# Performance work log

Measured on AMD Instinct MI355X. Metric: run time of the kernel, lower is better.

## Reference

```python
import jax, jax.numpy as jnp
import numpy as np

B = 8192
N_CLASSES = 1024
MARGIN = 0.1
THRESH = 0.5
SCALE_POS = 2.0
SCALE_NEG = 40.0
EPS = 1e-5


def setup_inputs() -> dict:
    key = jax.random.key(0)
    k1, k2 = jax.random.split(key)
    # cosine-similarity-like values in [-1, 1]
    sim_mat = jax.random.uniform(k1, (B, B), dtype=jnp.float32, minval=-1.0, maxval=1.0)
    labels = jax.random.randint(k2, (B,), 0, N_CLASSES, dtype=jnp.int64)
    return {"sim_mat": sim_mat, "labels": labels}


def reference(sim_mat, labels):
    # [B, B] pair masks
    same = labels[:, None] == labels[None, :]
    pos_mask = same & (sim_mat < 1.0 - EPS)        # positives, excluding self-sim ~ 1
    neg_mask = ~same

    # per-row hardest positive (min) / hardest negative (max); inf sentinels when empty
    min_pos = jnp.min(jnp.where(pos_mask, sim_mat, jnp.inf), axis=1)   # [B]
    max_neg = jnp.max(jnp.where(neg_mask, sim_mat, -jnp.inf), axis=1)  # [B]

    # pair mining: keep informative pairs only
    sel_neg = neg_mask & (sim_mat + MARGIN > min_pos[:, None])
    sel_pos = pos_mask & (sim_mat - MARGIN < max_neg[:, None])

    valid = jnp.any(sel_neg, axis=1) & jnp.any(sel_pos, axis=1)  # rows contributing to loss

    # masked soft-plus style logsumexp losses (sim bounded in [-1,1], exp is safe)
    pos_sum = jnp.sum(jnp.where(sel_pos, jnp.exp(-SCALE_POS * (sim_mat - THRESH)), 0.0), axis=1)
    neg_sum = jnp.sum(jnp.where(sel_neg, jnp.exp(SCALE_NEG * (sim_mat - THRESH)), 0.0), axis=1)
    pos_loss = jnp.log1p(pos_sum) / SCALE_POS
    neg_loss = jnp.log1p(neg_sum) / SCALE_NEG

    loss = jnp.sum(jnp.where(valid, pos_loss + neg_loss, 0.0)) / sim_mat.shape[0]
    return loss
```

## Files before the change

kernel.cpp:

```cpp
#include <hip/hip_runtime.h>
#include <math.h>

namespace {
constexpr int   kB        = 8192;
constexpr int   kBlock    = 256;
constexpr int   kVec      = 4;
constexpr int   kIters    = kB / (kBlock * kVec);
constexpr float kMargin   = 0.1f;
constexpr float kThresh   = 0.5f;
constexpr float kScalePos = 2.0f;
constexpr float kScaleNeg = 40.0f;
constexpr float kEps      = 1e-5f;
}

__global__ __launch_bounds__(kBlock, 4) void ms_loss_kernel(
    const float* __restrict__ sim,
    const int*   __restrict__ labels,
    float*       __restrict__ out)
{
  const int row  = blockIdx.x;
  const int tid  = threadIdx.x;
  const int wave = tid >> 6;
  const int lane = tid & 63;

  const int my_label = labels[row];
  const float* __restrict__ srow = sim + (size_t)row * kB;

  float4 v[kIters];
  #pragma unroll
  for (int k = 0; k < kIters; ++k) {
    v[k] = *reinterpret_cast<const float4*>(srow + k * (kBlock * kVec) + tid * kVec);
  }

  unsigned int same_mask = 0;
  #pragma unroll
  for (int k = 0; k < kIters; ++k) {
    const int4 l = *reinterpret_cast<const int4*>(labels + k * (kBlock * kVec) + tid * kVec);
    same_mask |= (unsigned)(l.x == my_label) << (k * 4 + 0);
    same_mask |= (unsigned)(l.y == my_label) << (k * 4 + 1);
    same_mask |= (unsigned)(l.z == my_label) << (k * 4 + 2);
    same_mask |= (unsigned)(l.w == my_label) << (k * 4 + 3);
  }

  float min_pos =  INFINITY;
  float max_neg = -INFINITY;
  #pragma unroll
  for (int k = 0; k < kIters; ++k) {
    const float xs[4] = {v[k].x, v[k].y, v[k].z, v[k].w};
    #pragma unroll
    for (int c = 0; c < 4; ++c) {
      const bool  same = (same_mask >> (k * 4 + c)) & 1u;
      const float x = xs[c];
      const float p = (same && x < 1.0f - kEps) ? x : INFINITY;
      const float n = same ? -INFINITY : x;
      min_pos = fminf(min_pos, p);
      max_neg = fmaxf(max_neg, n);
    }
  }

  #pragma unroll
  for (int off = 32; off > 0; off >>= 1) {
    min_pos = fminf(min_pos, __shfl_xor(min_pos, off, 64));
    max_neg = fmaxf(max_neg, __shfl_xor(max_neg, off, 64));
  }
  __shared__ float s_min[kBlock / 64];
  __shared__ float s_max[kBlock / 64];
  if (lane == 0) { s_min[wave] = min_pos; s_max[wave] = max_neg; }
  __syncthreads();
  min_pos = fminf(fminf(s_min[0], s_min[1]), fminf(s_min[2], s_min[3]));
  max_neg = fmaxf(fmaxf(s_max[0], s_max[1]), fmaxf(s_max[2], s_max[3]));

  float pos_sum = 0.0f, neg_sum = 0.0f;
  #pragma unroll
  for (int k = 0; k < kIters; ++k) {
    const float xs[4] = {v[k].x, v[k].y, v[k].z, v[k].w};
    #pragma unroll
    for (int c = 0; c < 4; ++c) {
      const bool  same = (same_mask >> (k * 4 + c)) & 1u;
      const float x = xs[c];
      const float a = same ? -kScalePos : kScaleNeg;
      const float e = __expf(a * (x - kThresh));
      const bool selp = same && (x < 1.0f - kEps) && (x - kMargin < max_neg);
      const bool seln = (!same) && (x + kMargin > min_pos);
      pos_sum += selp ? e : 0.0f;
      neg_sum += seln ? e : 0.0f;
    }
  }

  #pragma unroll
  for (int off = 32; off > 0; off >>= 1) {
    pos_sum += __shfl_xor(pos_sum, off, 64);
    neg_sum += __shfl_xor(neg_sum, off, 64);
  }
  __shared__ float s_pos[kBlock / 64];
  __shared__ float s_neg[kBlock / 64];
  if (lane == 0) { s_pos[wave] = pos_sum; s_neg[wave] = neg_sum; }
  __syncthreads();
  if (tid == 0) {
    pos_sum = (s_pos[0] + s_pos[1]) + (s_pos[2] + s_pos[3]);
    neg_sum = (s_neg[0] + s_neg[1]) + (s_neg[2] + s_neg[3]);
    if (pos_sum > 0.0f && neg_sum > 0.0f) {
      const float loss = log1pf(pos_sum) * (1.0f / kScalePos)
                       + log1pf(neg_sum) * (1.0f / kScaleNeg);
      atomicAdd(out, loss * (1.0f / (float)kB));
    }
  }
}

extern "C" void kernel_launch(void* const* d_in, const int* in_sizes, int n_in,
                              void* d_out, int out_size, void* d_ws, size_t ws_size,
                              hipStream_t stream) {
  const float* sim    = (const float*)d_in[0];
  const int*   labels = (const int*)d_in[1];
  float*       out    = (float*)d_out;

  hipMemsetAsync(d_out, 0, sizeof(float) * (size_t)out_size, stream);
  ms_loss_kernel<<<dim3(kB), dim3(kBlock), 0, stream>>>(sim, labels, out);
}
```

Measured before the change: 377.6 us.

## Process eight rows per block with double-buffered row prefetch

Each block now handles eight consecutive rows instead of one. It loads the column labels once and builds a same-label bitmask for every row up front. While the current row is reduced, the next row of the similarity matrix is loaded into a second register buffer, so load latency overlaps the min/max and exp passes. The per-row losses are summed in the block and written with one atomic, cutting global atomics eightfold. The costs are a higher register footprint from the two float4 buffers and a grid of only 1024 blocks, which may reduce occupancy and latency hiding.

After: 371.2 us. Within noise of the previous version (-1.7%).

```diff
diff --git a/kernel.cpp b/kernel.cpp
--- a/kernel.cpp
+++ b/kernel.cpp
@@ -5,7 +5,9 @@
 constexpr int   kB        = 8192;
 constexpr int   kBlock    = 256;
 constexpr int   kVec      = 4;
-constexpr int   kIters    = kB / (kBlock * kVec);
+constexpr int   kChunks   = kB / (kBlock * kVec);
+constexpr int   kRows     = 8;
+constexpr int   kGrid     = kB / kRows;
 constexpr float kMargin   = 0.1f;
 constexpr float kThresh   = 0.5f;
 constexpr float kScalePos = 2.0f;
@@ -18,92 +20,118 @@
     const int*   __restrict__ labels,
     float*       __restrict__ out)
 {
-  const int row  = blockIdx.x;
-  const int tid  = threadIdx.x;
-  const int wave = tid >> 6;
-  const int lane = tid & 63;
+  const int tid      = threadIdx.x;
+  const int wave     = tid >> 6;
+  const int lane     = tid & 63;
+  const int base_row = blockIdx.x * kRows;
 
-  const int my_label = labels[row];
-  const float* __restrict__ srow = sim + (size_t)row * kB;
+  int4 lab[kChunks];
+  #pragma unroll
+  for (int k = 0; k < kChunks; ++k)
+    lab[k] = *reinterpret_cast<const int4*>(labels + k * (kBlock * kVec) + tid * kVec);
 
-  float4 v[kIters];
+  unsigned int mask[kRows];
   #pragma unroll
-  for (int k = 0; k < kIters; ++k) {
-    v[k] = *reinterpret_cast<const float4*>(srow + k * (kBlock * kVec) + tid * kVec);
+  for (int r = 0; r < kRows; ++r) {
+    const int ml = labels[base_row + r];
+    unsigned int m = 0;
+    #pragma unroll
+    for (int k = 0; k < kChunks; ++k) {
+      m |= (unsigned)(lab[k].x == ml) << (k * 4 + 0);
+      m |= (unsigned)(lab[k].y == ml) << (k * 4 + 1);
+      m |= (unsigned)(lab[k].z == ml) << (k * 4 + 2);
+      m |= (unsigned)(lab[k].w == ml) << (k * 4 + 3);
+    }
+    mask[r] = m;
   }
 
-  unsigned int same_mask = 0;
-  #pragma unroll
-  for (int k = 0; k < kIters; ++k) {
-    const int4 l = *reinterpret_cast<const int4*>(labels + k * (kBlock * kVec) + tid * kVec);
-    same_mask |= (unsigned)(l.x == my_label) << (k * 4 + 0);
-    same_mask |= (unsigned)(l.y == my_label) << (k * 4 + 1);
-    same_mask |= (unsigned)(l.z == my_label) << (k * 4 + 2);
-    same_mask |= (unsigned)(l.w == my_label) << (k * 4 + 3);
+  float4 buf[2][kChunks];
+  {
+    const float* __restrict__ s0 = sim + (size_t)base_row * kB;
+    #pragma unroll
+    for (int k = 0; k < kChunks; ++k)
+      buf[0][k] = *reinterpret_cast<const float4*>(s0 + k * (kBlock * kVec) + tid * kVec);
   }
 
-  float min_pos =  INFINITY;
-  float max_neg = -INFINITY;
+  __shared__ float s_min[kBlock / 64];
+  __shared__ float s_max[kBlock / 64];
+  __shared__ float s_pos[kBlock / 64];
+  __shared__ float s_neg[kBlock / 64];
+
+  float block_loss = 0.0f;
+
   #pragma unroll
-  for (int k = 0; k < kIters; ++k) {
-    const float xs[4] = {v[k].x, v[k].y, v[k].z, v[k].w};
+  for (int r = 0; r < kRows; ++r) {
+    if (r + 1 < kRows) {
+      const float* __restrict__ sn = sim + (size_t)(base_row + r + 1) * kB;
+      #pragma unroll
+      for (int k = 0; k < kChunks; ++k)
+        buf[(r + 1) & 1][k] =
+            *reinterpret_cast<const float4*>(sn + k * (kBlock * kVec) + tid * kVec);
+    }
+
+    const unsigned int m = mask[r];
+
+    float min_pos =  INFINITY;
+    float max_neg = -INFINITY;
     #pragma unroll
-    for (int c = 0; c < 4; ++c) {
-      const bool  same = (same_mask >> (k * 4 + c)) & 1u;
-      const float x = xs[c];
-      const float p = (same && x < 1.0f - kEps) ? x : INFINITY;
-      const float n = same ? -INFINITY : x;
-      min_pos = fminf(min_pos, p);
-      max_neg = fmaxf(max_neg, n);
+    for (int k = 0; k < kChunks; ++k) {
+      const float4 v = buf[r & 1][k];
+      const float xs[4] = {v.x, v.y, v.z, v.w};
+      #pragma unroll
+      for (int c = 0; c < 4; ++c) {
+        const bool  same = (m >> (k * 4 + c)) & 1u;
+        const float x = xs[c];
+        min_pos = fminf(min_pos, (same && x < 1.0f - kEps) ? x : INFINITY);
+        max_neg = fmaxf(max_neg, same ? -INFINITY : x);
+      }
+    }
+    #pragma unroll
+    for (int off = 32; off > 0; off >>= 1) {
+      min_pos = fminf(min_pos, __shfl_xor(min_pos, off, 64));
+      max_neg = fmaxf(max_neg, __shfl_xor(max_neg, off, 64));
+    }
+    if (lane == 0) { s_min[wave] = min_pos; s_max[wave] = max_neg; }
+    __syncthreads();
+    min_pos = fminf(fminf(s_min[0], s_min[1]), fminf(s_min[2], s_min[3]));
+    max_neg = fmaxf(fmaxf(s_max[0], s_max[1]), fmaxf(s_max[2], s_max[3]));
+
+    float pos_sum = 0.0f, neg_sum = 0.0f;
+    #pragma unroll
+    for (int k = 0; k < kChunks; ++k) {
+      const float4 v = buf[r & 1][k];
+      const float xs[4] = {v.x, v.y, v.z, v.w};
+      #pragma unroll
+      for (int c = 0; c < 4; ++c) {
+        const bool  same = (m >> (k * 4 + c)) & 1u;
+        const float x = xs[c];
+        const float a = same ? -kScalePos : kScaleNeg;
+        const float e = __expf(a * (x - kThresh));
+        const bool selp = same && (x < 1.0f - kEps) && (x - kMargin < max_neg);
+        const bool seln = (!same) && (x + kMargin > min_pos);
+        pos_sum += selp ? e : 0.0f;
+        neg_sum += seln ? e : 0.0f;
+      }
+    }
+    #pragma unroll
+    for (int off = 32; off > 0; off >>= 1) {
+      pos_sum += __shfl_xor(pos_sum, off, 64);
+      neg_sum += __shfl_xor(neg_sum, off, 64);
+    }
+    if (lane == 0) { s_pos[wave] = pos_sum; s_neg[wave] = neg_sum; }
+    __syncthreads();
+    if (tid == 0) {
+      pos_sum = (s_pos[0] + s_pos[1]) + (s_pos[2] + s_pos[3]);
+      neg_sum = (s_neg[0] + s_neg[1]) + (s_neg[2] + s_neg[3]);
+      if (pos_sum > 0.0f && neg_sum > 0.0f) {
+        block_loss += log1pf(pos_sum) * (1.0f / kScalePos)
+                    + log1pf(neg_sum) * (1.0f / kScaleNeg);
+      }
     }
   }
 
-  #pragma unroll
-  for (int off = 32; off > 0; off >>= 1) {
-    min_pos = fminf(min_pos, __shfl_xor(min_pos, off, 64));
-    max_neg = fmaxf(max_neg, __shfl_xor(max_neg, off, 64));
-  }
-  __shared__ float s_min[kBlock / 64];
-  __shared__ float s_max[kBlock / 64];
-  if (lane == 0) { s_min[wave] = min_pos; s_max[wave] = max_neg; }
-  __syncthreads();
-  min_pos = fminf(fminf(s_min[0], s_min[1]), fminf(s_min[2], s_min[3]));
-  max_neg = fmaxf(fmaxf(s_max[0], s_max[1]), fmaxf(s_max[2], s_max[3]));
-
-  float pos_sum = 0.0f, neg_sum = 0.0f;
-  #pragma unroll
-  for (int k = 0; k < kIters; ++k) {
-    const float xs[4] = {v[k].x, v[k].y, v[k].z, v[k].w};
-    #pragma unroll
-    for (int c = 0; c < 4; ++c) {
-      const bool  same = (same_mask >> (k * 4 + c)) & 1u;
-      const float x = xs[c];
-      const float a = same ? -kScalePos : kScaleNeg;
-      const float e = __expf(a * (x - kThresh));
-      const bool selp = same && (x < 1.0f - kEps) && (x - kMargin < max_neg);
-      const bool seln = (!same) && (x + kMargin > min_pos);
-      pos_sum += selp ? e : 0.0f;
-      neg_sum += seln ? e : 0.0f;
-    }
-  }
-
-  #pragma unroll
-  for (int off = 32; off > 0; off >>= 1) {
-    pos_sum += __shfl_xor(pos_sum, off, 64);
-    neg_sum += __shfl_xor(neg_sum, off, 64);
-  }
-  __shared__ float s_pos[kBlock / 64];
-  __shared__ float s_neg[kBlock / 64];
-  if (lane == 0) { s_pos[wave] = pos_sum; s_neg[wave] = neg_sum; }
-  __syncthreads();
-  if (tid == 0) {
-    pos_sum = (s_pos[0] + s_pos[1]) + (s_pos[2] + s_pos[3]);
-    neg_sum = (s_neg[0] + s_neg[1]) + (s_neg[2] + s_neg[3]);
-    if (pos_sum > 0.0f && neg_sum > 0.0f) {
-      const float loss = log1pf(pos_sum) * (1.0f / kScalePos)
-                       + log1pf(neg_sum) * (1.0f / kScaleNeg);
-      atomicAdd(out, loss * (1.0f / (float)kB));
-    }
+  if (tid == 0 && block_loss != 0.0f) {
+    atomicAdd(out, block_loss * (1.0f / (float)kB));
   }
 }
 
@@ -115,5 +143,5 @@
   float*       out    = (float*)d_out;
 
   hipMemsetAsync(d_out, 0, sizeof(float) * (size_t)out_size, stream);
-  ms_loss_kernel<<<dim3(kB), dim3(kBlock), 0, stream>>>(sim, labels, out);
+  ms_loss_kernel<<<dim3(kGrid), dim3(kBlock), 0, stream>>>(sim, labels, out);
 }
```

## Map rows to single waves and replace atomics with two-stage reduction

Applied to the files above, without the earlier changes.

Each 64-lane wave now owns whole rows, two per wave, and holds the 8192-float row in 32 float4 registers, so block-level shared-memory reductions and syncthreads are gone. Per-wave partial losses go to workspace and a second single-block kernel sums them, which replaces the memset plus 8192 atomics. The cost is much higher register pressure (launch bounds lowered to 2) and less memory-level parallelism per row. It also depends on a workspace buffer and adds a second launch.

Measured after the change: 432.9 us. 14.6% more time.

```diff
diff --git a/kernel.cpp b/kernel.cpp
--- a/kernel.cpp
+++ b/kernel.cpp
@@ -2,10 +2,13 @@
 #include <math.h>
 
 namespace {
-constexpr int   kB        = 8192;
-constexpr int   kBlock    = 256;
-constexpr int   kVec      = 4;
-constexpr int   kIters    = kB / (kBlock * kVec);
+constexpr int   kB       = 8192;
+constexpr int   kBlock   = 256;
+constexpr int   kWaves   = kBlock / 64;
+constexpr int   kRPW     = 2;
+constexpr int   kGrid    = kB / (kWaves * kRPW);
+constexpr int   kChunks  = kB / (64 * 4);
+constexpr int   kNWaves  = kGrid * kWaves;
 constexpr float kMargin   = 0.1f;
 constexpr float kThresh   = 0.5f;
 constexpr float kScalePos = 2.0f;
@@ -13,98 +16,96 @@
 constexpr float kEps      = 1e-5f;
 }
 
-__global__ __launch_bounds__(kBlock, 4) void ms_loss_kernel(
+__global__ __launch_bounds__(kBlock, 2) void ms_rows_kernel(
     const float* __restrict__ sim,
     const int*   __restrict__ labels,
-    float*       __restrict__ out)
+    float*       __restrict__ ws)
 {
-  const int row  = blockIdx.x;
   const int tid  = threadIdx.x;
   const int wave = tid >> 6;
   const int lane = tid & 63;
+  const int wid  = blockIdx.x * kWaves + wave;
 
-  const int my_label = labels[row];
-  const float* __restrict__ srow = sim + (size_t)row * kB;
+  float wave_loss = 0.0f;
 
-  float4 v[kIters];
   #pragma unroll
-  for (int k = 0; k < kIters; ++k) {
-    v[k] = *reinterpret_cast<const float4*>(srow + k * (kBlock * kVec) + tid * kVec);
-  }
+  for (int rr = 0; rr < kRPW; ++rr) {
+    const int row = wid * kRPW + rr;
+    const int ml  = labels[row];
+    const float* __restrict__ srow = sim + (size_t)row * kB;
 
-  unsigned int same_mask = 0;
-  #pragma unroll
-  for (int k = 0; k < kIters; ++k) {
-    const int4 l = *reinterpret_cast<const int4*>(labels + k * (kBlock * kVec) + tid * kVec);
-    same_mask |= (unsigned)(l.x == my_label) << (k * 4 + 0);
-    same_mask |= (unsigned)(l.y == my_label) << (k * 4 + 1);
-    same_mask |= (unsigned)(l.z == my_label) << (k * 4 + 2);
-    same_mask |= (unsigned)(l.w == my_label) << (k * 4 + 3);
-  }
+    float4 buf[kChunks];
+    #pragma unroll
+    for (int k = 0; k < kChunks; ++k)
+      buf[k] = *reinterpret_cast<const float4*>(srow + k * 256 + lane * 4);
 
-  float min_pos =  INFINITY;
-  float max_neg = -INFINITY;
-  #pragma unroll
-  for (int k = 0; k < kIters; ++k) {
-    const float xs[4] = {v[k].x, v[k].y, v[k].z, v[k].w};
+    unsigned int msk[kChunks / 8] = {0, 0, 0, 0};
+    float min_pos =  INFINITY;
+    float max_neg = -INFINITY;
     #pragma unroll
-    for (int c = 0; c < 4; ++c) {
-      const bool  same = (same_mask >> (k * 4 + c)) & 1u;
-      const float x = xs[c];
-      const float p = (same && x < 1.0f - kEps) ? x : INFINITY;
-      const float n = same ? -INFINITY : x;
-      min_pos = fminf(min_pos, p);
-      max_neg = fmaxf(max_neg, n);
+    for (int k = 0; k < kChunks; ++k) {
+      const int4   l4 = *reinterpret_cast<const int4*>(labels + k * 256 + lane * 4);
+      const float4 v  = buf[k];
+      const float xs[4] = {v.x, v.y, v.z, v.w};
+      const int   ls[4] = {l4.x, l4.y, l4.z, l4.w};
+      #pragma unroll
+      for (int c = 0; c < 4; ++c) {
+        const bool  same = (ls[c] == ml);
+        msk[k >> 3] |= (unsigned)same << ((k & 7) * 4 + c);
+        const float x = xs[c];
+        min_pos = fminf(min_pos, (same && x < 1.0f - kEps) ? x : INFINITY);
+        max_neg = fmaxf(max_neg, same ? -INFINITY : x);
+      }
+    }
+    #pragma unroll
+    for (int off = 32; off > 0; off >>= 1) {
+      min_pos = fminf(min_pos, __shfl_xor(min_pos, off, 64));
+      max_neg = fmaxf(max_neg, __shfl_xor(max_neg, off, 64));
+    }
+
+    float ps = 0.0f, ns = 0.0f;
+    #pragma unroll
+    for (int k = 0; k < kChunks; ++k) {
+      const float4 v = buf[k];
+      const float xs[4] = {v.x, v.y, v.z, v.w};
+      #pragma unroll
+      for (int c = 0; c < 4; ++c) {
+        const bool  same = (msk[k >> 3] >> ((k & 7) * 4 + c)) & 1u;
+        const float x = xs[c];
+        const float a = same ? -kScalePos : kScaleNeg;
+        const float e = __expf(a * (x - kThresh));
+        ps += (same && x < 1.0f - kEps && x - kMargin < max_neg) ? e : 0.0f;
+        ns += (!same && x + kMargin > min_pos) ? e : 0.0f;
+      }
+    }
+    #pragma unroll
+    for (int off = 32; off > 0; off >>= 1) {
+      ps += __shfl_xor(ps, off, 64);
+      ns += __shfl_xor(ns, off, 64);
+    }
+    if (ps > 0.0f && ns > 0.0f) {
+      wave_loss += log1pf(ps) * (1.0f / kScalePos)
+                 + log1pf(ns) * (1.0f / kScaleNeg);
     }
   }
 
+  if (lane == 0) ws[wid] = wave_loss;
+}
+
+__global__ __launch_bounds__(256) void ms_reduce_kernel(
+    const float* __restrict__ ws, float* __restrict__ out)
+{
+  const int tid = threadIdx.x;
+  float s = 0.0f;
   #pragma unroll
-  for (int off = 32; off > 0; off >>= 1) {
-    min_pos = fminf(min_pos, __shfl_xor(min_pos, off, 64));
-    max_neg = fmaxf(max_neg, __shfl_xor(max_neg, off, 64));
-  }
-  __shared__ float s_min[kBlock / 64];
-  __shared__ float s_max[kBlock / 64];
-  if (lane == 0) { s_min[wave] = min_pos; s_max[wave] = max_neg; }
+  for (int i = tid; i < kNWaves; i += 256) s += ws[i];
+  #pragma unroll
+  for (int off = 32; off > 0; off >>= 1) s += __shfl_xor(s, off, 64);
+  __shared__ float sm[4];
+  if ((tid & 63) == 0) sm[tid >> 6] = s;
   __syncthreads();
-  min_pos = fminf(fminf(s_min[0], s_min[1]), fminf(s_min[2], s_min[3]));
-  max_neg = fmaxf(fmaxf(s_max[0], s_max[1]), fmaxf(s_max[2], s_max[3]));
-
-  float pos_sum = 0.0f, neg_sum = 0.0f;
-  #pragma unroll
-  for (int k = 0; k < kIters; ++k) {
-    const float xs[4] = {v[k].x, v[k].y, v[k].z, v[k].w};
-    #pragma unroll
-    for (int c = 0; c < 4; ++c) {
-      const bool  same = (same_mask >> (k * 4 + c)) & 1u;
-      const float x = xs[c];
-      const float a = same ? -kScalePos : kScaleNeg;
-      const float e = __expf(a * (x - kThresh));
-      const bool selp = same && (x < 1.0f - kEps) && (x - kMargin < max_neg);
-      const bool seln = (!same) && (x + kMargin > min_pos);
-      pos_sum += selp ? e : 0.0f;
-      neg_sum += seln ? e : 0.0f;
-    }
-  }
-
-  #pragma unroll
-  for (int off = 32; off > 0; off >>= 1) {
-    pos_sum += __shfl_xor(pos_sum, off, 64);
-    neg_sum += __shfl_xor(neg_sum, off, 64);
-  }
-  __shared__ float s_pos[kBlock / 64];
-  __shared__ float s_neg[kBlock / 64];
-  if (lane == 0) { s_pos[wave] = pos_sum; s_neg[wave] = neg_sum; }
-  __syncthreads();
-  if (tid == 0) {
-    pos_sum = (s_pos[0] + s_pos[1]) + (s_pos[2] + s_pos[3]);
-    neg_sum = (s_neg[0] + s_neg[1]) + (s_neg[2] + s_neg[3]);
-    if (pos_sum > 0.0f && neg_sum > 0.0f) {
-      const float loss = log1pf(pos_sum) * (1.0f / kScalePos)
-                       + log1pf(neg_sum) * (1.0f / kScaleNeg);
-      atomicAdd(out, loss * (1.0f / (float)kB));
-    }
-  }
+  if (tid == 0)
+    out[0] = (sm[0] + sm[1] + sm[2] + sm[3]) * (1.0f / (float)kB);
 }
 
 extern "C" void kernel_launch(void* const* d_in, const int* in_sizes, int n_in,
@@ -112,8 +113,9 @@
                               hipStream_t stream) {
   const float* sim    = (const float*)d_in[0];
   const int*   labels = (const int*)d_in[1];
+  float*       ws     = (float*)d_ws;
   float*       out    = (float*)d_out;
 
-  hipMemsetAsync(d_out, 0, sizeof(float) * (size_t)out_size, stream);
-  ms_loss_kernel<<<dim3(kB), dim3(kBlock), 0, stream>>>(sim, labels, out);
+  ms_rows_kernel<<<dim3(kGrid), dim3(kBlock), 0, stream>>>(sim, labels, ws);
+  ms_reduce_kernel<<<dim3(1), dim3(256), 0, stream>>>(ws, out);
 }
```
